# Optimization experiments

Hardware: AMD Instinct MI355X
Metric: run time of the kernel (lower is better)

The kernel has to match this reference:

```python
import jax, jax.numpy as jnp
import numpy as np

N_KNOTS = 16
DEGREE = 3
EPS = 1e-8


def make_knots(n_knots, degree):
    knots = np.zeros(n_knots, dtype=np.float32)
    for i in range(n_knots):
        if i <= degree:
            knots[i] = 0.0
        elif i >= n_knots - degree - 1:
            knots[i] = 1.0
        else:
            knots[i] = (i - degree) / (n_knots - 2 * degree - 1)
    return knots


def setup_inputs() -> dict:
    key = jax.random.key(0)
    k1, k2 = jax.random.split(key)
    x = jax.random.uniform(k1, (65536, 64), dtype=jnp.float32)
    control_points = jax.random.normal(k2, (64, 12, 64), dtype=jnp.float32)
    return {"x": x, "control_points": control_points}


def bspline_basis(x, knots_np, degree):
    # x: [B, D] in [0,1]; returns basis: [B, D, n_control_points]
    n_knots = knots_np.shape[0]
    n_intervals = n_knots - 1
    knots = jnp.asarray(knots_np)
    xe = x[..., None]  # [B, D, 1]
    left = knots[:-1]
    right = knots[1:]
    in_interval = (xe >= left) & (xe < right)
    last = (xe >= left[-1]) & (xe <= right[-1])  # include right endpoint of last interval
    basis = jnp.concatenate([in_interval[..., :-1], last], axis=-1).astype(x.dtype)
    for k in range(1, degree + 1):
        nb = n_intervals - k
        j = np.arange(nb)
        dL = knots_np[j + k] - knots_np[j]          # constants
        dR = knots_np[j + k + 1] - knots_np[j + 1]
        okL = np.abs(dL) > EPS
        okR = np.abs(dR) > EPS
        invL = jnp.asarray(np.where(okL, 1.0 / np.where(okL, dL, 1.0), 0.0).astype(np.float32))
        invR = jnp.asarray(np.where(okR, 1.0 / np.where(okR, dR, 1.0), 0.0).astype(np.float32))
        cL = (xe - knots[j]) * invL                 # [B, D, nb], zero where degenerate
        cR = (knots[j + k + 1] - xe) * invR
        basis = cL * basis[..., :nb] + cR * basis[..., 1:nb + 1]
    return basis


def reference(x, control_points):
    # x: [B, in_dim]; control_points: [in_dim, n_cp, out_dim]
    knots_np = make_knots(N_KNOTS, DEGREE)
    xc = jnp.clip(x, 0.0, 1.0)
    basis = bspline_basis(xc, knots_np, DEGREE)     # [B, in_dim, n_cp]
    return jnp.einsum('bic,ico->bo', basis, control_points)
```

## Files before the change

### kernel.cpp

```cpp
#include <hip/hip_runtime.h>


typedef short short8 __attribute__((ext_vector_type(8)));
typedef float f32x4 __attribute__((ext_vector_type(4)));
typedef unsigned u32x4 __attribute__((ext_vector_type(4)));

#define NSTEP 24
#define HSTEP 12
#define WAVES 8
#define THREADS (WAVES * 64)
#define RPW 32
#define RPB (WAVES * RPW)

static __device__ __forceinline__ unsigned bf16rne(float f) {
  unsigned u = __float_as_uint(f);
  return (u + 0x7FFFu + ((u >> 16) & 1u)) >> 16;
}

__global__ __launch_bounds__(256) void prep_wfrag(const float* __restrict__ cp,
                                                  unsigned* __restrict__ wfrag) {
  int id = blockIdx.x * 256 + threadIdx.x;
  int d  = id & 3;
  int l  = (id >> 2) & 63;
  int id2 = id >> 8;
  int p   = id2 / 48;
  int rem = id2 - p * 48;
  int nt  = rem / 12;
  int sl  = rem - nt * 12;
  int s   = p * 12 + sl;
  int g   = l >> 4;
  int o   = nt * 16 + (l & 15);
  int k0  = 192 * g + 8 * s + 2 * d;
  unsigned lo = bf16rne(cp[k0 * 64 + o]);
  unsigned hi = bf16rne(cp[(k0 + 1) * 64 + o]);
  wfrag[id] = lo | (hi << 16);
}

struct Pack6 { unsigned w0, w1, w2, w3, w4, w5; };

static __device__ __forceinline__ Pack6 eval_pack(float xi) {
  xi = fminf(fmaxf(xi, 0.0f), 1.0f);
  float t9 = xi * 9.0f;
  int jj = (int)t9;
  float validf = (jj <= 8) ? 1.0f : 0.0f;
  jj = (jj > 8) ? 8 : jj;
  float fj = (float)jj;
  float u  = t9 - fj;
  float omu = 1.0f - u;
  float c1  = fminf(fj, 1.0f);
  float c2  = fminf(fj, 2.0f);
  float rdj = 9.0f - fj;
  float d2p = fminf(rdj, 2.0f);
  float d3p = fminf(rdj, 3.0f);
  float invA = (jj == 0) ? 1.0f : 0.5f;
  float invB = (jj == 8) ? 1.0f : 0.5f;
  float invC = (jj == 0) ? 1.0f : ((jj == 1) ? 0.5f : (1.0f / 3.0f));
  float invD = (jj == 0 || jj == 8) ? 0.5f : (1.0f / 3.0f);
  float invE = (jj >= 7) ? ((jj == 8) ? 1.0f : 0.5f) : (1.0f / 3.0f);
  float xkm1 = u + c1, xkm2 = u + c2;
  float k2x = d2p - u, k3x = d3p - u;
  float t0 = omu * invA;
  float A0 = omu * t0;
  float s1 = xkm1 * t0;
  float t1 = u * invB;
  float A1 = fmaf(k2x, t1, s1);
  float A2 = u * t1;
  float u0 = A0 * invC;
  float B0 = omu * u0;
  float s2 = xkm2 * u0;
  float u1 = A1 * invD;
  float B1 = fmaf(k2x, u1, s2);
  float s3 = xkm1 * u1;
  float u2 = A2 * invE;
  float B2 = fmaf(k3x, u2, s3);
  float B3 = u * u2;
  B0 *= validf; B1 *= validf; B2 *= validf; B3 *= validf;

  unsigned b0 = bf16rne(B0), b1 = bf16rne(B1), b2 = bf16rne(B2), b3 = bf16rne(B3);
  unsigned p01 = b0 | (b1 << 16);
  unsigned p23 = b2 | (b3 << 16);
  unsigned O0 = p01 << 16;
  unsigned O1 = (p01 >> 16) | (p23 << 16);
  unsigned O2 = p23 >> 16;
  int e2 = jj >> 1;
  bool odd = (jj & 1) != 0;
#define VE(q) ((q == e2) ? p01 : ((q == e2 + 1) ? p23 : 0u))
#define VO(q) ((q == e2) ? O0 : ((q == e2 + 1) ? O1 : ((q == e2 + 2) ? O2 : 0u)))
  Pack6 r;
  r.w0 = odd ? VO(0) : VE(0);
  r.w1 = odd ? VO(1) : VE(1);
  r.w2 = odd ? VO(2) : VE(2);
  r.w3 = odd ? VO(3) : VE(3);
  r.w4 = odd ? VO(4) : VE(4);
  r.w5 = odd ? VO(5) : VE(5);
#undef VE
#undef VO
  return r;
}

__global__ __launch_bounds__(THREADS) void kan_mfma(const float* __restrict__ x,
                                                    const unsigned* __restrict__ wfrag,
                                                    float* __restrict__ out) {
  __shared__ u32x4 ldsB[4 * HSTEP * 64];
  const int tid  = threadIdx.x;
  const int lane = tid & 63;
  const int w    = tid >> 6;
  const int m = lane & 15, g = lane >> 4;
  const long row0 = ((long)blockIdx.x * WAVES + w) * RPW;

  float xr0[16], xr1[16];
  {
    const float4* p0 = (const float4*)(x + (row0 + m) * 64 + g * 16);
    const float4* p1 = (const float4*)(x + (row0 + 16 + m) * 64 + g * 16);
    #pragma unroll
    for (int q = 0; q < 4; ++q) {
      float4 v = p0[q];
      xr0[4 * q] = v.x; xr0[4 * q + 1] = v.y; xr0[4 * q + 2] = v.z; xr0[4 * q + 3] = v.w;
    }
    #pragma unroll
    for (int q = 0; q < 4; ++q) {
      float4 v = p1[q];
      xr1[4 * q] = v.x; xr1[4 * q + 1] = v.y; xr1[4 * q + 2] = v.z; xr1[4 * q + 3] = v.w;
    }
  }

  f32x4 acc[2][4];
  #pragma unroll
  for (int mt = 0; mt < 2; ++mt)
    #pragma unroll
    for (int nt = 0; nt < 4; ++nt)
      acc[mt][nt] = f32x4{0.0f, 0.0f, 0.0f, 0.0f};

  const u32x4* wsrc = (const u32x4*)wfrag;

  #pragma unroll
  for (int p = 0; p < 2; ++p) {
    if (p) __syncthreads();
    #pragma unroll
    for (int q = 0; q < (4 * HSTEP * 64) / THREADS; ++q)
      ldsB[q * THREADS + tid] = wsrc[p * 3072 + q * THREADS + tid];
    __syncthreads();

    #pragma unroll
    for (int tl = 0; tl < 4; ++tl) {
      const int t = p * 4 + tl;
      Pack6 aA = eval_pack(xr0[2 * t]);
      Pack6 aB = eval_pack(xr0[2 * t + 1]);
      Pack6 bA = eval_pack(xr1[2 * t]);
      Pack6 bB = eval_pack(xr1[2 * t + 1]);
      #pragma unroll
      for (int sub = 0; sub < 3; ++sub) {
        u32x4 qa, qb;
        if (sub == 0) {
          qa[0] = aA.w0; qa[1] = aA.w1; qa[2] = aA.w2; qa[3] = aA.w3;
          qb[0] = bA.w0; qb[1] = bA.w1; qb[2] = bA.w2; qb[3] = bA.w3;
        } else if (sub == 1) {
          qa[0] = aA.w4; qa[1] = aA.w5; qa[2] = aB.w0; qa[3] = aB.w1;
          qb[0] = bA.w4; qb[1] = bA.w5; qb[2] = bB.w0; qb[3] = bB.w1;
        } else {
          qa[0] = aB.w2; qa[1] = aB.w3; qa[2] = aB.w4; qa[3] = aB.w5;
          qb[0] = bB.w2; qb[1] = bB.w3; qb[2] = bB.w4; qb[3] = bB.w5;
        }
        short8 A0 = __builtin_bit_cast(short8, qa);
        short8 A1 = __builtin_bit_cast(short8, qb);
        const int sl = 3 * tl + sub;
        #pragma unroll
        for (int nt = 0; nt < 4; ++nt) {
          u32x4 bq = ldsB[(nt * HSTEP + sl) * 64 + lane];
          short8 B = __builtin_bit_cast(short8, bq);
          acc[0][nt] = __builtin_amdgcn_mfma_f32_16x16x32_bf16(A0, B, acc[0][nt], 0, 0, 0);
          acc[1][nt] = __builtin_amdgcn_mfma_f32_16x16x32_bf16(A1, B, acc[1][nt], 0, 0, 0);
        }
      }
    }
  }

  #pragma unroll
  for (int mt = 0; mt < 2; ++mt)
    #pragma unroll
    for (int nt = 0; nt < 4; ++nt)
      #pragma unroll
      for (int j = 0; j < 4; ++j)
        out[(row0 + mt * 16 + g * 4 + j) * 64 + nt * 16 + m] = acc[mt][nt][j];
}

extern "C" void kernel_launch(void* const* d_in, const int* in_sizes, int n_in,
                              void* d_out, int out_size, void* d_ws, size_t ws_size,
                              hipStream_t stream) {
  const float* x  = (const float*)d_in[0];
  const float* cp = (const float*)d_in[1];
  float* out = (float*)d_out;
  unsigned* wfrag = (unsigned*)d_ws;

  hipLaunchKernelGGL(prep_wfrag, dim3(96), dim3(256), 0, stream, cp, wfrag);
  const int rows = in_sizes[0] / 64;
  hipLaunchKernelGGL(kan_mfma, dim3(rows / RPB), dim3(THREADS), 0, stream,
                     x, wfrag, out);
}
```

Before: 91.87 us.

## Fuse weight bf16 packing into main kernel and halve rows per wave

Drops the separate prep kernel. Each block now converts control points to bf16 MFMA fragments directly into shared memory. Block size doubles to 16 waves with 16 rows per wave, so each wave issues one MFMA per B fragment instead of two. This removes one kernel launch and the workspace round-trip. In exchange, every block does strided global reads and conversion of the weights, and B fragment reuse per LDS read is halved.

```diff
diff --git a/kernel.cpp b/kernel.cpp
--- a/kernel.cpp
+++ b/kernel.cpp
@@ -5,35 +5,15 @@
 typedef float f32x4 __attribute__((ext_vector_type(4)));
 typedef unsigned u32x4 __attribute__((ext_vector_type(4)));
 
-#define NSTEP 24
+#define WAVES 16
+#define THREADS (WAVES * 64)
+#define RPW 16
+#define RPB (WAVES * RPW)
 #define HSTEP 12
-#define WAVES 8
-#define THREADS (WAVES * 64)
-#define RPW 32
-#define RPB (WAVES * RPW)
 
 static __device__ __forceinline__ unsigned bf16rne(float f) {
   unsigned u = __float_as_uint(f);
   return (u + 0x7FFFu + ((u >> 16) & 1u)) >> 16;
-}
-
-__global__ __launch_bounds__(256) void prep_wfrag(const float* __restrict__ cp,
-                                                  unsigned* __restrict__ wfrag) {
-  int id = blockIdx.x * 256 + threadIdx.x;
-  int d  = id & 3;
-  int l  = (id >> 2) & 63;
-  int id2 = id >> 8;
-  int p   = id2 / 48;
-  int rem = id2 - p * 48;
-  int nt  = rem / 12;
-  int sl  = rem - nt * 12;
-  int s   = p * 12 + sl;
-  int g   = l >> 4;
-  int o   = nt * 16 + (l & 15);
-  int k0  = 192 * g + 8 * s + 2 * d;
-  unsigned lo = bf16rne(cp[k0 * 64 + o]);
-  unsigned hi = bf16rne(cp[(k0 + 1) * 64 + o]);
-  wfrag[id] = lo | (hi << 16);
 }
 
 struct Pack6 { unsigned w0, w1, w2, w3, w4, w5; };
@@ -98,90 +78,84 @@
   return r;
 }
 
-__global__ __launch_bounds__(THREADS) void kan_mfma(const float* __restrict__ x,
-                                                    const unsigned* __restrict__ wfrag,
-                                                    float* __restrict__ out) {
+__global__ __launch_bounds__(THREADS, 4) void kan_mfma(const float* __restrict__ x,
+                                                       const float* __restrict__ cp,
+                                                       float* __restrict__ out) {
   __shared__ u32x4 ldsB[4 * HSTEP * 64];
   const int tid  = threadIdx.x;
   const int lane = tid & 63;
   const int w    = tid >> 6;
   const int m = lane & 15, g = lane >> 4;
-  const long row0 = ((long)blockIdx.x * WAVES + w) * RPW;
+  const long row0 = (long)blockIdx.x * RPB + w * RPW;
 
-  float xr0[16], xr1[16];
+  float xr[16];
   {
     const float4* p0 = (const float4*)(x + (row0 + m) * 64 + g * 16);
-    const float4* p1 = (const float4*)(x + (row0 + 16 + m) * 64 + g * 16);
     #pragma unroll
     for (int q = 0; q < 4; ++q) {
       float4 v = p0[q];
-      xr0[4 * q] = v.x; xr0[4 * q + 1] = v.y; xr0[4 * q + 2] = v.z; xr0[4 * q + 3] = v.w;
-    }
-    #pragma unroll
-    for (int q = 0; q < 4; ++q) {
-      float4 v = p1[q];
-      xr1[4 * q] = v.x; xr1[4 * q + 1] = v.y; xr1[4 * q + 2] = v.z; xr1[4 * q + 3] = v.w;
+      xr[4 * q] = v.x; xr[4 * q + 1] = v.y; xr[4 * q + 2] = v.z; xr[4 * q + 3] = v.w;
     }
   }
 
-  f32x4 acc[2][4];
+  f32x4 acc[4];
   #pragma unroll
-  for (int mt = 0; mt < 2; ++mt)
-    #pragma unroll
-    for (int nt = 0; nt < 4; ++nt)
-      acc[mt][nt] = f32x4{0.0f, 0.0f, 0.0f, 0.0f};
-
-  const u32x4* wsrc = (const u32x4*)wfrag;
+  for (int nt = 0; nt < 4; ++nt) acc[nt] = f32x4{0.0f, 0.0f, 0.0f, 0.0f};
 
   #pragma unroll
   for (int p = 0; p < 2; ++p) {
     if (p) __syncthreads();
+
     #pragma unroll
-    for (int q = 0; q < (4 * HSTEP * 64) / THREADS; ++q)
-      ldsB[q * THREADS + tid] = wsrc[p * 3072 + q * THREADS + tid];
+    for (int q = 0; q < (4 * HSTEP * 64) / THREADS; ++q) {
+      int sidx = q * THREADS + tid;
+      int l2   = sidx & 63;
+      int idx2 = sidx >> 6;
+      int nt   = idx2 / HSTEP;
+      int sl   = idx2 - nt * HSTEP;
+      int gg   = l2 >> 4;
+      int o    = nt * 16 + (l2 & 15);
+      int kb   = 192 * gg + 8 * (p * HSTEP + sl);
+      const float* src = cp + o;
+      u32x4 v;
+      #pragma unroll
+      for (int d = 0; d < 4; ++d) {
+        unsigned lo = bf16rne(src[(kb + 2 * d) * 64]);
+        unsigned hi = bf16rne(src[(kb + 2 * d + 1) * 64]);
+        v[d] = lo | (hi << 16);
+      }
+      ldsB[sidx] = v;
+    }
     __syncthreads();
 
     #pragma unroll
     for (int tl = 0; tl < 4; ++tl) {
       const int t = p * 4 + tl;
-      Pack6 aA = eval_pack(xr0[2 * t]);
-      Pack6 aB = eval_pack(xr0[2 * t + 1]);
-      Pack6 bA = eval_pack(xr1[2 * t]);
-      Pack6 bB = eval_pack(xr1[2 * t + 1]);
+      Pack6 aA = eval_pack(xr[2 * t]);
+      Pack6 aB = eval_pack(xr[2 * t + 1]);
       #pragma unroll
       for (int sub = 0; sub < 3; ++sub) {
-        u32x4 qa, qb;
-        if (sub == 0) {
-          qa[0] = aA.w0; qa[1] = aA.w1; qa[2] = aA.w2; qa[3] = aA.w3;
-          qb[0] = bA.w0; qb[1] = bA.w1; qb[2] = bA.w2; qb[3] = bA.w3;
-        } else if (sub == 1) {
-          qa[0] = aA.w4; qa[1] = aA.w5; qa[2] = aB.w0; qa[3] = aB.w1;
-          qb[0] = bA.w4; qb[1] = bA.w5; qb[2] = bB.w0; qb[3] = bB.w1;
-        } else {
-          qa[0] = aB.w2; qa[1] = aB.w3; qa[2] = aB.w4; qa[3] = aB.w5;
-          qb[0] = bB.w2; qb[1] = bB.w3; qb[2] = bB.w4; qb[3] = bB.w5;
-        }
-        short8 A0 = __builtin_bit_cast(short8, qa);
-        short8 A1 = __builtin_bit_cast(short8, qb);
+        u32x4 qa;
+        if (sub == 0)      { qa[0] = aA.w0; qa[1] = aA.w1; qa[2] = aA.w2; qa[3] = aA.w3; }
+        else if (sub == 1) { qa[0] = aA.w4; qa[1] = aA.w5; qa[2] = aB.w0; qa[3] = aB.w1; }
+        else               { qa[0] = aB.w2; qa[1] = aB.w3; qa[2] = aB.w4; qa[3] = aB.w5; }
+        short8 A = __builtin_bit_cast(short8, qa);
         const int sl = 3 * tl + sub;
         #pragma unroll
         for (int nt = 0; nt < 4; ++nt) {
           u32x4 bq = ldsB[(nt * HSTEP + sl) * 64 + lane];
           short8 B = __builtin_bit_cast(short8, bq);
-          acc[0][nt] = __builtin_amdgcn_mfma_f32_16x16x32_bf16(A0, B, acc[0][nt], 0, 0, 0);
-          acc[1][nt] = __builtin_amdgcn_mfma_f32_16x16x32_bf16(A1, B, acc[1][nt], 0, 0, 0);
+          acc[nt] = __builtin_amdgcn_mfma_f32_16x16x32_bf16(A, B, acc[nt], 0, 0, 0);
         }
       }
     }
   }
 
   #pragma unroll
-  for (int mt = 0; mt < 2; ++mt)
+  for (int nt = 0; nt < 4; ++nt)
     #pragma unroll
-    for (int nt = 0; nt < 4; ++nt)
-      #pragma unroll
-      for (int j = 0; j < 4; ++j)
-        out[(row0 + mt * 16 + g * 4 + j) * 64 + nt * 16 + m] = acc[mt][nt][j];
+    for (int j = 0; j < 4; ++j)
+      out[(row0 + g * 4 + j) * 64 + nt * 16 + m] = acc[nt][j];
 }
 
 extern "C" void kernel_launch(void* const* d_in, const int* in_sizes, int n_in,
@@ -190,10 +164,7 @@
   const float* x  = (const float*)d_in[0];
   const float* cp = (const float*)d_in[1];
   float* out = (float*)d_out;
-  unsigned* wfrag = (unsigned*)d_ws;
-
-  hipLaunchKernelGGL(prep_wfrag, dim3(96), dim3(256), 0, stream, cp, wfrag);
   const int rows = in_sizes[0] / 64;
   hipLaunchKernelGGL(kan_mfma, dim3(rows / RPB), dim3(THREADS), 0, stream,
-                     x, wfrag, out);
+                     x, cp, out);
 }
```

Measured after the change: 87.54 us. -4.7%, faster.

## Split output columns across wave pairs and load weights directly from global

Applied to the files above, without the earlier changes.

Removes the shared-memory staging of weight fragments and barriers, loading B fragments per lane from global (L2-resident) memory instead. Each wave now handles half the output column tiles for a 32-row block, with smaller 256-thread blocks and four times as many blocks. This shortens per-wave MFMA chains and removes sync, but duplicates the B-spline basis evaluation across the two waves sharing rows and adds global load latency.

```diff
diff --git a/kernel.cpp b/kernel.cpp
--- a/kernel.cpp
+++ b/kernel.cpp
@@ -5,12 +5,7 @@
 typedef float f32x4 __attribute__((ext_vector_type(4)));
 typedef unsigned u32x4 __attribute__((ext_vector_type(4)));
 
-#define NSTEP 24
-#define HSTEP 12
-#define WAVES 8
-#define THREADS (WAVES * 64)
-#define RPW 32
-#define RPB (WAVES * RPW)
+#define THREADS 256
 
 static __device__ __forceinline__ unsigned bf16rne(float f) {
   unsigned u = __float_as_uint(f);
@@ -23,14 +18,11 @@
   int d  = id & 3;
   int l  = (id >> 2) & 63;
   int id2 = id >> 8;
-  int p   = id2 / 48;
-  int rem = id2 - p * 48;
-  int nt  = rem / 12;
-  int sl  = rem - nt * 12;
-  int s   = p * 12 + sl;
-  int g   = l >> 4;
-  int o   = nt * 16 + (l & 15);
-  int k0  = 192 * g + 8 * s + 2 * d;
+  int nt = id2 / 24;
+  int s  = id2 - nt * 24;
+  int g  = l >> 4;
+  int o  = nt * 16 + (l & 15);
+  int k0 = 192 * g + 8 * s + 2 * d;
   unsigned lo = bf16rne(cp[k0 * 64 + o]);
   unsigned hi = bf16rne(cp[(k0 + 1) * 64 + o]);
   wfrag[id] = lo | (hi << 16);
@@ -98,15 +90,15 @@
   return r;
 }
 
-__global__ __launch_bounds__(THREADS) void kan_mfma(const float* __restrict__ x,
-                                                    const unsigned* __restrict__ wfrag,
-                                                    float* __restrict__ out) {
-  __shared__ u32x4 ldsB[4 * HSTEP * 64];
+__global__ __launch_bounds__(THREADS, 4) void kan_mfma(const float* __restrict__ x,
+                                                       const unsigned* __restrict__ wfrag,
+                                                       float* __restrict__ out) {
   const int tid  = threadIdx.x;
   const int lane = tid & 63;
   const int w    = tid >> 6;
   const int m = lane & 15, g = lane >> 4;
-  const long row0 = ((long)blockIdx.x * WAVES + w) * RPW;
+  const long row0 = (long)blockIdx.x * 64 + (w >> 1) * 32;
+  const int  ntb  = (w & 1) * 2;
 
   float xr0[16], xr1[16];
   {
@@ -124,64 +116,58 @@
     }
   }
 
-  f32x4 acc[2][4];
+  f32x4 acc[2][2];
   #pragma unroll
   for (int mt = 0; mt < 2; ++mt)
     #pragma unroll
-    for (int nt = 0; nt < 4; ++nt)
-      acc[mt][nt] = f32x4{0.0f, 0.0f, 0.0f, 0.0f};
+    for (int ntl = 0; ntl < 2; ++ntl)
+      acc[mt][ntl] = f32x4{0.0f, 0.0f, 0.0f, 0.0f};
 
-  const u32x4* wsrc = (const u32x4*)wfrag;
+  const u32x4* wf4 = (const u32x4*)wfrag;
 
   #pragma unroll
-  for (int p = 0; p < 2; ++p) {
-    if (p) __syncthreads();
+  for (int q = 0; q < 8; ++q) {
+    u32x4 bq0[3], bq1[3];
     #pragma unroll
-    for (int q = 0; q < (4 * HSTEP * 64) / THREADS; ++q)
-      ldsB[q * THREADS + tid] = wsrc[p * 3072 + q * THREADS + tid];
-    __syncthreads();
-
+    for (int sub = 0; sub < 3; ++sub) {
+      bq0[sub] = wf4[((ntb + 0) * 24 + 3 * q + sub) * 64 + lane];
+      bq1[sub] = wf4[((ntb + 1) * 24 + 3 * q + sub) * 64 + lane];
+    }
+    Pack6 aA = eval_pack(xr0[2 * q]);
+    Pack6 aB = eval_pack(xr0[2 * q + 1]);
+    Pack6 bA = eval_pack(xr1[2 * q]);
+    Pack6 bB = eval_pack(xr1[2 * q + 1]);
     #pragma unroll
-    for (int tl = 0; tl < 4; ++tl) {
-      const int t = p * 4 + tl;
-      Pack6 aA = eval_pack(xr0[2 * t]);
-      Pack6 aB = eval_pack(xr0[2 * t + 1]);
-      Pack6 bA = eval_pack(xr1[2 * t]);
-      Pack6 bB = eval_pack(xr1[2 * t + 1]);
-      #pragma unroll
-      for (int sub = 0; sub < 3; ++sub) {
-        u32x4 qa, qb;
-        if (sub == 0) {
-          qa[0] = aA.w0; qa[1] = aA.w1; qa[2] = aA.w2; qa[3] = aA.w3;
-          qb[0] = bA.w0; qb[1] = bA.w1; qb[2] = bA.w2; qb[3] = bA.w3;
-        } else if (sub == 1) {
-          qa[0] = aA.w4; qa[1] = aA.w5; qa[2] = aB.w0; qa[3] = aB.w1;
-          qb[0] = bA.w4; qb[1] = bA.w5; qb[2] = bB.w0; qb[3] = bB.w1;
-        } else {
-          qa[0] = aB.w2; qa[1] = aB.w3; qa[2] = aB.w4; qa[3] = aB.w5;
-          qb[0] = bB.w2; qb[1] = bB.w3; qb[2] = bB.w4; qb[3] = bB.w5;
-        }
-        short8 A0 = __builtin_bit_cast(short8, qa);
-        short8 A1 = __builtin_bit_cast(short8, qb);
-        const int sl = 3 * tl + sub;
-        #pragma unroll
-        for (int nt = 0; nt < 4; ++nt) {
-          u32x4 bq = ldsB[(nt * HSTEP + sl) * 64 + lane];
-          short8 B = __builtin_bit_cast(short8, bq);
-          acc[0][nt] = __builtin_amdgcn_mfma_f32_16x16x32_bf16(A0, B, acc[0][nt], 0, 0, 0);
-          acc[1][nt] = __builtin_amdgcn_mfma_f32_16x16x32_bf16(A1, B, acc[1][nt], 0, 0, 0);
-        }
+    for (int sub = 0; sub < 3; ++sub) {
+      u32x4 qa, qb;
+      if (sub == 0) {
+        qa[0] = aA.w0; qa[1] = aA.w1; qa[2] = aA.w2; qa[3] = aA.w3;
+        qb[0] = bA.w0; qb[1] = bA.w1; qb[2] = bA.w2; qb[3] = bA.w3;
+      } else if (sub == 1) {
+        qa[0] = aA.w4; qa[1] = aA.w5; qa[2] = aB.w0; qa[3] = aB.w1;
+        qb[0] = bA.w4; qb[1] = bA.w5; qb[2] = bB.w0; qb[3] = bB.w1;
+      } else {
+        qa[0] = aB.w2; qa[1] = aB.w3; qa[2] = aB.w4; qa[3] = aB.w5;
+        qb[0] = bB.w2; qb[1] = bB.w3; qb[2] = bB.w4; qb[3] = bB.w5;
       }
+      short8 A0 = __builtin_bit_cast(short8, qa);
+      short8 A1 = __builtin_bit_cast(short8, qb);
+      short8 Bf0 = __builtin_bit_cast(short8, bq0[sub]);
+      short8 Bf1 = __builtin_bit_cast(short8, bq1[sub]);
+      acc[0][0] = __builtin_amdgcn_mfma_f32_16x16x32_bf16(A0, Bf0, acc[0][0], 0, 0, 0);
+      acc[1][0] = __builtin_amdgcn_mfma_f32_16x16x32_bf16(A1, Bf0, acc[1][0], 0, 0, 0);
+      acc[0][1] = __builtin_amdgcn_mfma_f32_16x16x32_bf16(A0, Bf1, acc[0][1], 0, 0, 0);
+      acc[1][1] = __builtin_amdgcn_mfma_f32_16x16x32_bf16(A1, Bf1, acc[1][1], 0, 0, 0);
     }
   }
 
   #pragma unroll
   for (int mt = 0; mt < 2; ++mt)
     #pragma unroll
-    for (int nt = 0; nt < 4; ++nt)
+    for (int ntl = 0; ntl < 2; ++ntl)
       #pragma unroll
       for (int j = 0; j < 4; ++j)
-        out[(row0 + mt * 16 + g * 4 + j) * 64 + nt * 16 + m] = acc[mt][nt][j];
+        out[(row0 + mt * 16 + g * 4 + j) * 64 + (ntb + ntl) * 16 + m] = acc[mt][ntl][j];
 }
 
 extern "C" void kernel_launch(void* const* d_in, const int* in_sizes, int n_in,
@@ -194,6 +180,6 @@
 
   hipLaunchKernelGGL(prep_wfrag, dim3(96), dim3(256), 0, stream, cp, wfrag);
   const int rows = in_sizes[0] / 64;
-  hipLaunchKernelGGL(kan_mfma, dim3(rows / RPB), dim3(THREADS), 0, stream,
+  hipLaunchKernelGGL(kan_mfma, dim3(rows / 64), dim3(THREADS), 0, stream,
                      x, wfrag, out);
 }
```

New measurement: 100.8 us. +9.7%, slower.
